# Optimization experiments

Hardware: AMD Instinct MI355X
Metric: run time of the kernel (lower is better)

## Reference

```python
import jax, jax.numpy as jnp
import numpy as np

SEQ, BATCH, HIDDEN = 2048, 2, 2048
NUM_HEADS = 16
HEAD_DIM = HIDDEN // NUM_HEADS  # 128


def setup_inputs() -> dict:
    key = jax.random.key(0)
    k1, k2, k3, k4, k5 = jax.random.split(key, 5)
    scale = 1.0 / np.sqrt(HIDDEN)
    return {
        "hidden_states": jax.random.normal(k1, (SEQ, BATCH, HIDDEN), dtype=jnp.float32),
        "w_qkv": jax.random.normal(k2, (3 * HIDDEN, HIDDEN), dtype=jnp.float32) * scale,
        "b_qkv": jax.random.normal(k3, (3 * HIDDEN,), dtype=jnp.float32) * 0.01,
        "w_dense": jax.random.normal(k4, (HIDDEN, HIDDEN), dtype=jnp.float32) * scale,
        "b_dense": jax.random.normal(k5, (HIDDEN,), dtype=jnp.float32) * 0.01,
    }


def reference(hidden_states, w_qkv, b_qkv, w_dense, b_dense):
    s, b, H = hidden_states.shape
    nh, d = NUM_HEADS, HEAD_DIM
    norm_factor = jnp.asarray(np.sqrt(d), dtype=hidden_states.dtype)

    # QKV projection: [s, b, 3H] -> [s, b, nh, 3d] -> chunk into q, k, v
    mixed = hidden_states @ w_qkv.T + b_qkv
    mixed = mixed.reshape(s, b, nh, 3 * d)
    q, k, v = jnp.split(mixed, 3, axis=-1)  # each [s, b, nh, d]

    # Causal scaled dot-product attention, materializing [b, nh, sq, sk]
    scores = jnp.einsum("sbhd,tbhd->bhst", q, k) / norm_factor
    causal = jnp.tril(jnp.ones((s, s), dtype=bool))  # [sq, sk]
    scores = jnp.where(causal[None, None, :, :], scores, jnp.asarray(-10000.0, scores.dtype))
    probs = jax.nn.softmax(scores, axis=-1)

    # Context: [s, b, nh, d] -> [s, b, H]
    ctx = jnp.einsum("bhst,tbhd->sbhd", probs, v).reshape(s, b, H)

    # Output projection
    return ctx @ w_dense.T + b_dense
```

## Files before the change

kernel.cpp:

```cpp
#include <hip/hip_runtime.h>
#include <stdint.h>
#include <stddef.h>

#define SEQ   2048
#define BATCH 2
#define HID   2048
#define NH    16
#define HD    128
#define MTOT  (SEQ*BATCH)
#define NQKV  (3*HID)
#define KDIM  HID
#define LOG2E 1.4426950408889634f

typedef short  bf16x8 __attribute__((ext_vector_type(8)));
typedef float  f32x4  __attribute__((ext_vector_type(4)));

__device__ __forceinline__ unsigned short f2bf(float f) {
  union { float f; uint32_t u; } a; a.f = f;
  uint32_t r = a.u + 0x7fffu + ((a.u >> 16) & 1u);
  return (unsigned short)(r >> 16);
}

__device__ __forceinline__ f32x4 mfma16(bf16x8 a, bf16x8 b, f32x4 c) {
  return __builtin_amdgcn_mfma_f32_16x16x32_bf16(a, b, c, 0, 0, 0);
}

__device__ __forceinline__ void gl_lds16(const unsigned short* g, unsigned short* l) {
  __builtin_amdgcn_global_load_lds(
      (const __attribute__((address_space(1))) void*)g,
      (__attribute__((address_space(3))) void*)l, 16, 0, 0);
}

__global__ void cvt_f32_bf16(const float* __restrict__ in,
                             unsigned short* __restrict__ out, int n4) {
  int i = blockIdx.x * blockDim.x + threadIdx.x;
  int stride = gridDim.x * blockDim.x;
  for (; i < n4; i += stride) {
    float4 f = reinterpret_cast<const float4*>(in)[i];
    ushort4 o;
    o.x = f2bf(f.x); o.y = f2bf(f.y); o.z = f2bf(f.z); o.w = f2bf(f.w);
    reinterpret_cast<ushort4*>(out)[i] = o;
  }
}

__global__ __launch_bounds__(256) void transpose_v(
    const unsigned short* __restrict__ V, unsigned short* __restrict__ Vt) {
  __shared__ unsigned short tile[64][72];
  const int t  = threadIdx.x;
  const int bh = blockIdx.z;
  const int s0 = blockIdx.x * 64;
  const int d0 = blockIdx.y * 64;
  const size_t vb = (size_t)bh * SEQ * HD;
  const size_t tb = (size_t)bh * HD * SEQ;
#pragma unroll
  for (int p = 0; p < 2; ++p) {
    int r = p * 32 + (t >> 3);
    *(uint4*)&tile[r][(t & 7) * 8] =
        *(const uint4*)&V[vb + (size_t)(s0 + r) * HD + d0 + (t & 7) * 8];
  }
  __syncthreads();
#pragma unroll
  for (int p = 0; p < 2; ++p) {
    int dr = p * 32 + (t >> 3);
    int sc = (t & 7) * 8;
    unsigned short tmp[8];
#pragma unroll
    for (int e = 0; e < 8; ++e) tmp[e] = tile[sc + e][dr];
    *(uint4*)&Vt[tb + (size_t)(d0 + dr) * SEQ + s0 + sc] = *(const uint4*)tmp;
  }
}

__global__ __launch_bounds__(256, 3) void qkv_gemm(
    const unsigned short* __restrict__ A,
    const unsigned short* __restrict__ B,
    const float* __restrict__ bias,
    unsigned short* __restrict__ Qo,
    unsigned short* __restrict__ Ko,
    unsigned short* __restrict__ Vo)
{
  __shared__ unsigned short Ash[128 * 32];
  __shared__ unsigned short Bsh[128 * 32];
  const int t = threadIdx.x, l = t & 63, w = t >> 6;
  const int wm = w >> 1, wn = w & 1;
  int nwg = gridDim.x * gridDim.y;
  int id  = blockIdx.y * gridDim.x + blockIdx.x;
  int swz = (id & 7) * (nwg >> 3) + (id >> 3);
  const int m0 = (swz / gridDim.x) * 128, n0 = (swz % gridDim.x) * 128;
  const int fr = l & 15, fg = l >> 4;

  f32x4 acc[4][4] = {};
  for (int kk = 0; kk < KDIM / 32; ++kk) {
    const unsigned short* Akk = A + kk * 32;
    const unsigned short* Bkk = B + kk * 32;
#pragma unroll
    for (int i = 0; i < 2; ++i) {
      int ch  = w * 2 + i;
      int row = ch * 16 + (l >> 2);
      int c16 = (l & 3) ^ (row & 3);
      gl_lds16(Akk + (size_t)(m0 + row) * KDIM + c16 * 8, &Ash[ch * 512]);
      gl_lds16(Bkk + (size_t)(n0 + row) * KDIM + c16 * 8, &Bsh[ch * 512]);
    }
    __syncthreads();
    bf16x8 af[4], bfr[4];
#pragma unroll
    for (int m = 0; m < 4; ++m) {
      int row = wm * 64 + m * 16 + fr;
      af[m] = *(const bf16x8*)&Ash[row * 32 + ((fg ^ (row & 3)) * 8)];
    }
#pragma unroll
    for (int n = 0; n < 4; ++n) {
      int row = wn * 64 + n * 16 + fr;
      bfr[n] = *(const bf16x8*)&Bsh[row * 32 + ((fg ^ (row & 3)) * 8)];
    }
#pragma unroll
    for (int m = 0; m < 4; ++m)
#pragma unroll
      for (int n = 0; n < 4; ++n)
        acc[m][n] = mfma16(af[m], bfr[n], acc[m][n]);
    __syncthreads();
  }

  const int g4 = (l >> 4) * 4;
#pragma unroll
  for (int n = 0; n < 4; ++n) {
    int ncol = n0 + wn * 64 + n * 16 + fr;
    float bv = bias[ncol];
    int head = ncol / 384;
    int rem  = ncol - head * 384;
    int wi   = rem >> 7;
    int d    = rem & 127;
    unsigned short* dst = (wi == 0) ? Qo : ((wi == 1) ? Ko : Vo);
#pragma unroll
    for (int m = 0; m < 4; ++m) {
#pragma unroll
      for (int j = 0; j < 4; ++j) {
        int r = m0 + wm * 64 + m * 16 + g4 + j;
        int s = r >> 1, bb = r & 1;
        float val = acc[m][n][j] + bv;
        if (wi == 0) val *= 0.08838834764831845f;
        dst[(((size_t)(bb * NH + head)) * SEQ + s) * HD + d] = f2bf(val);
      }
    }
  }
}

__global__ __launch_bounds__(256, 2) void attn_fwd(
    const unsigned short* __restrict__ Q,
    const unsigned short* __restrict__ K,
    const unsigned short* __restrict__ Vt,
    unsigned short* __restrict__ ctx)
{
  __shared__ unsigned short Ksh[2][64 * 128];
  __shared__ unsigned short Vsh[2][128 * 64];
  __shared__ unsigned short Psh[4][16 * 72];
  const int t = threadIdx.x, l = t & 63, w = t >> 6;
  int nwg = gridDim.x * gridDim.y;
  int id  = blockIdx.y * gridDim.x + blockIdx.x;
  int swz = (id & 7) * (nwg >> 3) + (id >> 3);
  const int pair = swz & 15;
  const int bh   = swz >> 4;
  const int qtA = pair, qtB = 31 - pair;
  const int fr = l & 15, fg = l >> 4;
  const size_t base  = (size_t)bh * SEQ * HD;
  const size_t vbase = (size_t)bh * HD * SEQ;

#define STAGE(BUF, KT) do {                                                   \
    const unsigned short* Kt_ = K + base + (size_t)((KT) * 64) * HD;          \
    _Pragma("unroll")                                                         \
    for (int i_ = 0; i_ < 4; ++i_) {                                          \
      int ch_  = w * 4 + i_;                                                  \
      int row_ = ch_ * 4 + (l >> 4);                                          \
      int c16_ = (l & 15) ^ (row_ & 7);                                       \
      gl_lds16(Kt_ + (size_t)row_ * HD + c16_ * 8, &Ksh[BUF][ch_ * 512]);     \
    }                                                                         \
    const unsigned short* Vg_ = Vt + vbase + (KT) * 64;                       \
    _Pragma("unroll")                                                         \
    for (int i_ = 0; i_ < 4; ++i_) {                                          \
      int ch_  = w * 4 + i_;                                                  \
      int row_ = ch_ * 8 + (l >> 3);                                          \
      int c16_ = (l & 7) ^ (row_ & 7);                                        \
      gl_lds16(Vg_ + (size_t)row_ * SEQ + c16_ * 8, &Vsh[BUF][ch_ * 512]);    \
    }                                                                         \
  } while (0)

#define COMPUTE_TILE(QF, OACC, MROW, LROW, QT) do {                           \
    f32x4 sacc[4] = {};                                                       \
    _Pragma("unroll")                                                         \
    for (int c_ = 0; c_ < 4; ++c_) {                                          \
      _Pragma("unroll")                                                       \
      for (int n_ = 0; n_ < 4; ++n_) {                                        \
        int krow = n_ * 16 + fr;                                              \
        int g_   = (c_ * 4 + fg) ^ (krow & 7);                                \
        bf16x8 kf = *(const bf16x8*)&Ksh[buf][krow * 128 + g_ * 8];           \
        sacc[n_] = mfma16(QF[c_], kf, sacc[n_]);                              \
      }                                                                       \
    }                                                                         \
    if (kt == (QT)) {                                                         \
      _Pragma("unroll")                                                       \
      for (int n_ = 0; n_ < 4; ++n_)                                          \
        _Pragma("unroll")                                                     \
        for (int j_ = 0; j_ < 4; ++j_)                                        \
          if (n_ * 16 + fr > w * 16 + fg * 4 + j_) sacc[n_][j_] = -1e30f;     \
    }                                                                         \
    float tm_[4];                                                             \
    _Pragma("unroll")                                                         \
    for (int j_ = 0; j_ < 4; ++j_) {                                          \
      float v0 = fmaxf(fmaxf(sacc[0][j_], sacc[1][j_]),                       \
                       fmaxf(sacc[2][j_], sacc[3][j_]));                      \
      v0 = fmaxf(v0, __shfl_xor(v0, 1));                                      \
      v0 = fmaxf(v0, __shfl_xor(v0, 2));                                      \
      v0 = fmaxf(v0, __shfl_xor(v0, 4));                                      \
      v0 = fmaxf(v0, __shfl_xor(v0, 8));                                      \
      tm_[j_] = v0;                                                           \
    }                                                                         \
    float sc_[4], ps_[4];                                                     \
    _Pragma("unroll")                                                         \
    for (int j_ = 0; j_ < 4; ++j_) {                                          \
      float mn_ = fmaxf(MROW[j_], tm_[j_]);                                   \
      sc_[j_] = exp2f((MROW[j_] - mn_) * LOG2E);                              \
      MROW[j_] = mn_;                                                         \
      ps_[j_] = 0.f;                                                          \
    }                                                                         \
    _Pragma("unroll")                                                         \
    for (int n_ = 0; n_ < 4; ++n_)                                            \
      _Pragma("unroll")                                                       \
      for (int j_ = 0; j_ < 4; ++j_) {                                        \
        float p_ = exp2f((sacc[n_][j_] - MROW[j_]) * LOG2E);                  \
        sacc[n_][j_] = p_;                                                    \
        ps_[j_] += p_;                                                        \
      }                                                                       \
    _Pragma("unroll")                                                         \
    for (int j_ = 0; j_ < 4; ++j_) {                                          \
      float s_ = ps_[j_];                                                     \
      s_ += __shfl_xor(s_, 1);                                                \
      s_ += __shfl_xor(s_, 2);                                                \
      s_ += __shfl_xor(s_, 4);                                                \
      s_ += __shfl_xor(s_, 8);                                                \
      LROW[j_] = LROW[j_] * sc_[j_] + s_;                                     \
    }                                                                         \
    _Pragma("unroll")                                                         \
    for (int n_ = 0; n_ < 8; ++n_)                                            \
      _Pragma("unroll")                                                       \
      for (int j_ = 0; j_ < 4; ++j_)                                          \
        OACC[n_][j_] *= sc_[j_];                                              \
    _Pragma("unroll")                                                         \
    for (int n_ = 0; n_ < 4; ++n_)                                            \
      _Pragma("unroll")                                                       \
      for (int j_ = 0; j_ < 4; ++j_)                                          \
        Psh[w][(fg * 4 + j_) * 72 + n_ * 16 + fr] = f2bf(sacc[n_][j_]);       \
    _Pragma("unroll")                                                         \
    for (int ks_ = 0; ks_ < 2; ++ks_) {                                       \
      bf16x8 pf = *(const bf16x8*)&Psh[w][fr * 72 + ks_ * 32 + fg * 8];       \
      _Pragma("unroll")                                                       \
      for (int n_ = 0; n_ < 8; ++n_) {                                        \
        int vrow = n_ * 16 + fr;                                              \
        int g_   = (ks_ * 4 + fg) ^ (vrow & 7);                               \
        bf16x8 vf = *(const bf16x8*)&Vsh[buf][vrow * 64 + g_ * 8];            \
        OACC[n_] = mfma16(pf, vf, OACC[n_]);                                  \
      }                                                                       \
    }                                                                         \
  } while (0)

  bf16x8 qfA[4], qfB[4];
  {
    const unsigned short* qpA = Q + base + (size_t)(qtA * 64 + w * 16 + fr) * HD + fg * 8;
    const unsigned short* qpB = Q + base + (size_t)(qtB * 64 + w * 16 + fr) * HD + fg * 8;
#pragma unroll
    for (int c = 0; c < 4; ++c) {
      qfA[c] = *(const bf16x8*)(qpA + c * 32);
      qfB[c] = *(const bf16x8*)(qpB + c * 32);
    }
  }
  f32x4 oaccA[8] = {}, oaccB[8] = {};
  float mA[4] = {-1e30f, -1e30f, -1e30f, -1e30f};
  float mB[4] = {-1e30f, -1e30f, -1e30f, -1e30f};
  float lA[4] = {0.f, 0.f, 0.f, 0.f};
  float lB[4] = {0.f, 0.f, 0.f, 0.f};

  STAGE(0, 0);
  __syncthreads();
  int buf = 0;
  for (int kt = 0; kt <= qtB; ++kt) {
    if (kt < qtB) STAGE(buf ^ 1, kt + 1);
    COMPUTE_TILE(qfB, oaccB, mB, lB, qtB);
    if (kt <= qtA) COMPUTE_TILE(qfA, oaccA, mA, lA, qtA);
    __syncthreads();
    buf ^= 1;
  }

  const int bb = bh >> 4, h = bh & 15;
#define WRITE_CTX(OACC, LROW, QT) do {                                        \
    _Pragma("unroll")                                                         \
    for (int n_ = 0; n_ < 8; ++n_)                                            \
      _Pragma("unroll")                                                       \
      for (int j_ = 0; j_ < 4; ++j_) {                                        \
        int qrow = (QT) * 64 + w * 16 + fg * 4 + j_;                          \
        float val = OACC[n_][j_] / LROW[j_];                                  \
        ctx[((size_t)(qrow * BATCH + bb)) * HID + h * HD + n_ * 16 + fr] =    \
            f2bf(val);                                                        \
      }                                                                       \
  } while (0)
  WRITE_CTX(oaccA, lA, qtA);
  WRITE_CTX(oaccB, lB, qtB);
#undef STAGE
#undef COMPUTE_TILE
#undef WRITE_CTX
}

__global__ __launch_bounds__(256, 3) void dense_gemm(
    const unsigned short* __restrict__ A,
    const unsigned short* __restrict__ B,
    const float* __restrict__ bias,
    float* __restrict__ out)
{
  __shared__ unsigned short Ash[128 * 32];
  __shared__ unsigned short Bsh[128 * 32];
  const int t = threadIdx.x, l = t & 63, w = t >> 6;
  const int wm = w >> 1, wn = w & 1;
  int nwg = gridDim.x * gridDim.y;
  int id  = blockIdx.y * gridDim.x + blockIdx.x;
  int swz = (id & 7) * (nwg >> 3) + (id >> 3);
  const int m0 = (swz / gridDim.x) * 128, n0 = (swz % gridDim.x) * 128;
  const int fr = l & 15, fg = l >> 4;

  f32x4 acc[4][4] = {};
  for (int kk = 0; kk < KDIM / 32; ++kk) {
    const unsigned short* Akk = A + kk * 32;
    const unsigned short* Bkk = B + kk * 32;
#pragma unroll
    for (int i = 0; i < 2; ++i) {
      int ch  = w * 2 + i;
      int row = ch * 16 + (l >> 2);
      int c16 = (l & 3) ^ (row & 3);
      gl_lds16(Akk + (size_t)(m0 + row) * KDIM + c16 * 8, &Ash[ch * 512]);
      gl_lds16(Bkk + (size_t)(n0 + row) * KDIM + c16 * 8, &Bsh[ch * 512]);
    }
    __syncthreads();
    bf16x8 af[4], bfr[4];
#pragma unroll
    for (int m = 0; m < 4; ++m) {
      int row = wm * 64 + m * 16 + fr;
      af[m] = *(const bf16x8*)&Ash[row * 32 + ((fg ^ (row & 3)) * 8)];
    }
#pragma unroll
    for (int n = 0; n < 4; ++n) {
      int row = wn * 64 + n * 16 + fr;
      bfr[n] = *(const bf16x8*)&Bsh[row * 32 + ((fg ^ (row & 3)) * 8)];
    }
#pragma unroll
    for (int m = 0; m < 4; ++m)
#pragma unroll
      for (int n = 0; n < 4; ++n)
        acc[m][n] = mfma16(af[m], bfr[n], acc[m][n]);
    __syncthreads();
  }

  const int g4 = (l >> 4) * 4;
#pragma unroll
  for (int n = 0; n < 4; ++n) {
    int ncol = n0 + wn * 64 + n * 16 + fr;
    float bv = bias[ncol];
#pragma unroll
    for (int m = 0; m < 4; ++m) {
#pragma unroll
      for (int j = 0; j < 4; ++j) {
        int r = m0 + wm * 64 + m * 16 + g4 + j;
        out[(size_t)r * HID + ncol] = acc[m][n][j] + bv;
      }
    }
  }
}

extern "C" void kernel_launch(void* const* d_in, const int* in_sizes, int n_in,
                              void* d_out, int out_size, void* d_ws, size_t ws_size,
                              hipStream_t stream) {
  const float* hs      = (const float*)d_in[0];
  const float* w_qkv   = (const float*)d_in[1];
  const float* b_qkv   = (const float*)d_in[2];
  const float* w_dense = (const float*)d_in[3];
  const float* b_dense = (const float*)d_in[4];
  float* out = (float*)d_out;

  unsigned short* hsb = (unsigned short*)d_ws;
  unsigned short* wqb = hsb + (size_t)MTOT * HID;
  unsigned short* wdb = wqb + (size_t)NQKV * HID;
  unsigned short* q   = wdb + (size_t)HID * HID;
  unsigned short* k   = q   + (size_t)MTOT * HID;
  unsigned short* v   = k   + (size_t)MTOT * HID;
  unsigned short* ctx = v   + (size_t)MTOT * HID;
  unsigned short* vt  = hsb;

  cvt_f32_bf16<<<2048, 256, 0, stream>>>(hs,      hsb, (MTOT * HID) / 4);
  cvt_f32_bf16<<<2048, 256, 0, stream>>>(w_qkv,   wqb, (NQKV * HID) / 4);
  cvt_f32_bf16<<<1024, 256, 0, stream>>>(w_dense, wdb, (HID * HID) / 4);

  qkv_gemm<<<dim3(NQKV / 128, MTOT / 128), 256, 0, stream>>>(hsb, wqb, b_qkv, q, k, v);
  transpose_v<<<dim3(SEQ / 64, HD / 64, BATCH * NH), 256, 0, stream>>>(v, vt);
  attn_fwd<<<dim3(16, 32), 256, 0, stream>>>(q, k, vt, ctx);
  dense_gemm<<<dim3(HID / 128, MTOT / 128), 256, 0, stream>>>(ctx, wdb, b_dense, out);
}
```

Before: 308.1 us.

## Pipeline GEMMs with 4-stage LDS ring, 256x128 tiles and 512-thread blocks

```diff
diff --git a/kernel.cpp b/kernel.cpp
--- a/kernel.cpp
+++ b/kernel.cpp
@@ -12,6 +12,9 @@
 #define KDIM  HID
 #define LOG2E 1.4426950408889634f
 
+#define BK      32
+#define NTILES  (KDIM/BK)
+
 typedef short  bf16x8 __attribute__((ext_vector_type(8)));
 typedef float  f32x4  __attribute__((ext_vector_type(4)));
 
@@ -70,7 +73,64 @@
   }
 }
 
-__global__ __launch_bounds__(256, 3) void qkv_gemm(
+
+#define GEMM_PRE()                                                            \
+  const int t = threadIdx.x, l = t & 63, w = t >> 6;                          \
+  const int wm = w >> 1, wn = w & 1;                                          \
+  const int fr = l & 15, fg = l >> 4;                                         \
+  const int sg = ((l & 3) ^ ((l >> 2) & 3)) * 8;                              \
+  const int sr = (w * 16) + (l >> 2);                                         \
+  const unsigned short* Aw = A + (size_t)(m0 + sr) * KDIM + sg;               \
+  const unsigned short* Bw = B + (size_t)(n0 + sr) * KDIM + sg;               \
+  const int aoff = (wm * 64 + fr) * 32 + ((fg ^ (fr & 3)) * 8);               \
+  const int boff = 8192 + (wn * 64 + fr) * 32 + ((fg ^ (fr & 3)) * 8);        \
+  f32x4 acc[4][4] = {};
+
+#define STAGE_AB(KT) do {                                                     \
+    unsigned short* dst = sm[(KT) & 3];                                       \
+    const unsigned short* ap = Aw + (size_t)(KT) * BK;                        \
+    gl_lds16(ap,                      &dst[w * 512]);                         \
+    gl_lds16(ap + (size_t)128 * KDIM, &dst[4096 + w * 512]);                  \
+    gl_lds16(Bw + (size_t)(KT) * BK,  &dst[8192 + w * 512]);                  \
+  } while (0)
+
+#define GEMM_BODY(KT, VM, DOSTAGE) do {                                       \
+    const unsigned short* sb = sm[(KT) & 3];                                  \
+    if (DOSTAGE) STAGE_AB((KT) + 3);                                          \
+    bf16x8 af[4], bf[4];                                                      \
+    _Pragma("unroll")                                                         \
+    for (int m_ = 0; m_ < 4; ++m_)                                            \
+      af[m_] = *(const bf16x8*)&sb[aoff + m_ * 512];                          \
+    _Pragma("unroll")                                                         \
+    for (int n_ = 0; n_ < 4; ++n_)                                            \
+      bf[n_] = *(const bf16x8*)&sb[boff + n_ * 512];                          \
+    asm volatile("s_waitcnt vmcnt(" #VM ")" ::: "memory");                    \
+    asm volatile("s_barrier" ::: "memory");                                   \
+    asm volatile("s_waitcnt lgkmcnt(0)" ::: "memory");                        \
+    __builtin_amdgcn_sched_barrier(0);                                        \
+    __builtin_amdgcn_s_setprio(1);                                            \
+    _Pragma("unroll")                                                         \
+    for (int m_ = 0; m_ < 4; ++m_)                                            \
+      _Pragma("unroll")                                                       \
+      for (int n_ = 0; n_ < 4; ++n_)                                          \
+        acc[m_][n_] = mfma16(af[m_], bf[n_], acc[m_][n_]);                    \
+    __builtin_amdgcn_sched_barrier(0);                                        \
+    __builtin_amdgcn_s_setprio(0);                                            \
+    asm volatile("s_barrier" ::: "memory");                                   \
+  } while (0)
+
+#define GEMM_MAIN()                                                           \
+  STAGE_AB(0); STAGE_AB(1); STAGE_AB(2);                                      \
+  asm volatile("s_waitcnt vmcnt(6)" ::: "memory");                            \
+  asm volatile("s_barrier" ::: "memory");                                     \
+  _Pragma("unroll 1")                                                         \
+  for (int kt = 0; kt < NTILES - 3; ++kt)                                     \
+    GEMM_BODY(kt, 6, 1);                                                      \
+  GEMM_BODY(NTILES - 3, 3, 0);                                                \
+  GEMM_BODY(NTILES - 2, 0, 0);                                                \
+  GEMM_BODY(NTILES - 1, 0, 0);
+
+__global__ __launch_bounds__(512, 1) void qkv_gemm(
     const unsigned short* __restrict__ A,
     const unsigned short* __restrict__ B,
     const float* __restrict__ bias,
@@ -78,49 +138,14 @@
     unsigned short* __restrict__ Ko,
     unsigned short* __restrict__ Vo)
 {
-  __shared__ unsigned short Ash[128 * 32];
-  __shared__ unsigned short Bsh[128 * 32];
-  const int t = threadIdx.x, l = t & 63, w = t >> 6;
-  const int wm = w >> 1, wn = w & 1;
-  int nwg = gridDim.x * gridDim.y;
-  int id  = blockIdx.y * gridDim.x + blockIdx.x;
-  int swz = (id & 7) * (nwg >> 3) + (id >> 3);
-  const int m0 = (swz / gridDim.x) * 128, n0 = (swz % gridDim.x) * 128;
-  const int fr = l & 15, fg = l >> 4;
-
-  f32x4 acc[4][4] = {};
-  for (int kk = 0; kk < KDIM / 32; ++kk) {
-    const unsigned short* Akk = A + kk * 32;
-    const unsigned short* Bkk = B + kk * 32;
-#pragma unroll
-    for (int i = 0; i < 2; ++i) {
-      int ch  = w * 2 + i;
-      int row = ch * 16 + (l >> 2);
-      int c16 = (l & 3) ^ (row & 3);
-      gl_lds16(Akk + (size_t)(m0 + row) * KDIM + c16 * 8, &Ash[ch * 512]);
-      gl_lds16(Bkk + (size_t)(n0 + row) * KDIM + c16 * 8, &Bsh[ch * 512]);
-    }
-    __syncthreads();
-    bf16x8 af[4], bfr[4];
-#pragma unroll
-    for (int m = 0; m < 4; ++m) {
-      int row = wm * 64 + m * 16 + fr;
-      af[m] = *(const bf16x8*)&Ash[row * 32 + ((fg ^ (row & 3)) * 8)];
-    }
-#pragma unroll
-    for (int n = 0; n < 4; ++n) {
-      int row = wn * 64 + n * 16 + fr;
-      bfr[n] = *(const bf16x8*)&Bsh[row * 32 + ((fg ^ (row & 3)) * 8)];
-    }
-#pragma unroll
-    for (int m = 0; m < 4; ++m)
-#pragma unroll
-      for (int n = 0; n < 4; ++n)
-        acc[m][n] = mfma16(af[m], bfr[n], acc[m][n]);
-    __syncthreads();
-  }
-
-  const int g4 = (l >> 4) * 4;
+  __shared__ unsigned short sm[4][12288];
+  int id  = blockIdx.x;
+  int swz = (id & 7) * (gridDim.x >> 3) + (id >> 3);
+  const int m0 = (swz / 48) * 256, n0 = (swz % 48) * 128;
+  GEMM_PRE();
+  GEMM_MAIN();
+
+  const int g4 = fg * 4;
 #pragma unroll
   for (int n = 0; n < 4; ++n) {
     int ncol = n0 + wn * 64 + n * 16 + fr;
@@ -139,6 +164,35 @@
         float val = acc[m][n][j] + bv;
         if (wi == 0) val *= 0.08838834764831845f;
         dst[(((size_t)(bb * NH + head)) * SEQ + s) * HD + d] = f2bf(val);
+      }
+    }
+  }
+}
+
+__global__ __launch_bounds__(512, 1) void dense_gemm(
+    const unsigned short* __restrict__ A,
+    const unsigned short* __restrict__ B,
+    const float* __restrict__ bias,
+    float* __restrict__ out)
+{
+  __shared__ unsigned short sm[4][12288];
+  int id  = blockIdx.x;
+  int swz = (id & 7) * (gridDim.x >> 3) + (id >> 3);
+  const int m0 = (swz / 16) * 256, n0 = (swz % 16) * 128;
+  GEMM_PRE();
+  GEMM_MAIN();
+
+  const int g4 = fg * 4;
+#pragma unroll
+  for (int n = 0; n < 4; ++n) {
+    int ncol = n0 + wn * 64 + n * 16 + fr;
+    float bv = bias[ncol];
+#pragma unroll
+    for (int m = 0; m < 4; ++m) {
+#pragma unroll
+      for (int j = 0; j < 4; ++j) {
+        int r = m0 + wm * 64 + m * 16 + g4 + j;
+        out[(size_t)r * HID + ncol] = acc[m][n][j] + bv;
       }
     }
   }
@@ -307,70 +361,6 @@
 #undef WRITE_CTX
 }
 
-__global__ __launch_bounds__(256, 3) void dense_gemm(
-    const unsigned short* __restrict__ A,
-    const unsigned short* __restrict__ B,
-    const float* __restrict__ bias,
-    float* __restrict__ out)
-{
-  __shared__ unsigned short Ash[128 * 32];
-  __shared__ unsigned short Bsh[128 * 32];
-  const int t = threadIdx.x, l = t & 63, w = t >> 6;
-  const int wm = w >> 1, wn = w & 1;
-  int nwg = gridDim.x * gridDim.y;
-  int id  = blockIdx.y * gridDim.x + blockIdx.x;
-  int swz = (id & 7) * (nwg >> 3) + (id >> 3);
-  const int m0 = (swz / gridDim.x) * 128, n0 = (swz % gridDim.x) * 128;
-  const int fr = l & 15, fg = l >> 4;
-
-  f32x4 acc[4][4] = {};
-  for (int kk = 0; kk < KDIM / 32; ++kk) {
-    const unsigned short* Akk = A + kk * 32;
-    const unsigned short* Bkk = B + kk * 32;
-#pragma unroll
-    for (int i = 0; i < 2; ++i) {
-      int ch  = w * 2 + i;
-      int row = ch * 16 + (l >> 2);
-      int c16 = (l & 3) ^ (row & 3);
-      gl_lds16(Akk + (size_t)(m0 + row) * KDIM + c16 * 8, &Ash[ch * 512]);
-      gl_lds16(Bkk + (size_t)(n0 + row) * KDIM + c16 * 8, &Bsh[ch * 512]);
-    }
-    __syncthreads();
-    bf16x8 af[4], bfr[4];
-#pragma unroll
-    for (int m = 0; m < 4; ++m) {
-      int row = wm * 64 + m * 16 + fr;
-      af[m] = *(const bf16x8*)&Ash[row * 32 + ((fg ^ (row & 3)) * 8)];
-    }
-#pragma unroll
-    for (int n = 0; n < 4; ++n) {
-      int row = wn * 64 + n * 16 + fr;
-      bfr[n] = *(const bf16x8*)&Bsh[row * 32 + ((fg ^ (row & 3)) * 8)];
-    }
-#pragma unroll
-    for (int m = 0; m < 4; ++m)
-#pragma unroll
-      for (int n = 0; n < 4; ++n)
-        acc[m][n] = mfma16(af[m], bfr[n], acc[m][n]);
-    __syncthreads();
-  }
-
-  const int g4 = (l >> 4) * 4;
-#pragma unroll
-  for (int n = 0; n < 4; ++n) {
-    int ncol = n0 + wn * 64 + n * 16 + fr;
-    float bv = bias[ncol];
-#pragma unroll
-    for (int m = 0; m < 4; ++m) {
-#pragma unroll
-      for (int j = 0; j < 4; ++j) {
-        int r = m0 + wm * 64 + m * 16 + g4 + j;
-        out[(size_t)r * HID + ncol] = acc[m][n][j] + bv;
-      }
-    }
-  }
-}
-
 extern "C" void kernel_launch(void* const* d_in, const int* in_sizes, int n_in,
                               void* d_out, int out_size, void* d_ws, size_t ws_size,
                               hipStream_t stream) {
@@ -394,8 +384,8 @@
   cvt_f32_bf16<<<2048, 256, 0, stream>>>(w_qkv,   wqb, (NQKV * HID) / 4);
   cvt_f32_bf16<<<1024, 256, 0, stream>>>(w_dense, wdb, (HID * HID) / 4);
 
-  qkv_gemm<<<dim3(NQKV / 128, MTOT / 128), 256, 0, stream>>>(hsb, wqb, b_qkv, q, k, v);
+  qkv_gemm<<<dim3((MTOT / 256) * (NQKV / 128)), 512, 0, stream>>>(hsb, wqb, b_qkv, q, k, v);
   transpose_v<<<dim3(SEQ / 64, HD / 64, BATCH * NH), 256, 0, stream>>>(v, vt);
   attn_fwd<<<dim3(16, 32), 256, 0, stream>>>(q, k, vt, ctx);
-  dense_gemm<<<dim3(HID / 128, MTOT / 128), 256, 0, stream>>>(ctx, wdb, b_dense, out);
-}
+  dense_gemm<<<dim3((MTOT / 256) * (HID / 128)), 512, 0, stream>>>(ctx, wdb, b_dense, out);
+}
```

Result: faster. 293.0 us (-4.9%).
